# Kernel optimization log

Hardware: AMD Instinct MI355X
Metric: run time of the kernel (lower is better)

## Reference

```python
import jax, jax.numpy as jnp
import numpy as np

N, C, H, W = 64, 64, 8, 8   # batch, channels (img_net_out_dim), feature-map HxW
E = 256                      # ques_rnn_hidden_dim
G = 512                      # rn_g_dim
FD = 512                     # rn_f_dim
GIN = 2 * (C + 2) + E        # g-MLP input dim = 388
NUM_CLASSES = 2


def _lin(key, din, dout):
    # kaiming-uniform-like init for a Linear stored as (in, out)
    bound = float(np.sqrt(6.0 / din))
    w = jax.random.uniform(key, (din, dout), minval=-bound, maxval=bound, dtype=jnp.float32)
    b = jnp.zeros((dout,), dtype=jnp.float32)
    return w, b


def setup_inputs() -> dict:
    key = jax.random.key(0)
    ks = jax.random.split(key, 9)
    img = jax.random.normal(ks[0], (N, C, H, W), dtype=jnp.float32)
    ques = jax.random.normal(ks[1], (N, E), dtype=jnp.float32)
    g_w1, g_b1 = _lin(ks[2], GIN, G)
    g_w2, g_b2 = _lin(ks[3], G, G)
    g_w3, g_b3 = _lin(ks[4], G, G)
    g_w4, g_b4 = _lin(ks[5], G, G)
    f_w1, f_b1 = _lin(ks[6], G, FD)
    f_w2, f_b2 = _lin(ks[7], FD, FD)
    f_w3, f_b3 = _lin(ks[8], FD, NUM_CLASSES)
    return dict(img=img, ques=ques,
                g_w1=g_w1, g_b1=g_b1, g_w2=g_w2, g_b2=g_b2,
                g_w3=g_w3, g_b3=g_b3, g_w4=g_w4, g_b4=g_b4,
                f_w1=f_w1, f_b1=f_b1, f_w2=f_w2, f_b2=f_b2,
                f_w3=f_w3, f_b3=f_b3)


def _img_to_pairs(img, ques):
    # img: (n, c, h, w), ques: (n, e) -> pairs: (n, hw*hw, 2*(c+2)+e)
    n, c, h, w = img.shape
    hw = h * w
    cells = img.reshape(n, c, hw)
    idx = jnp.arange(hw)
    loc = jnp.stack([idx // w, idx % w], axis=0).astype(img.dtype)  # (2, hw)
    cells = jnp.concatenate([cells, jnp.broadcast_to(loc[None], (n, 2, hw))], axis=1)
    feats = cells.transpose(0, 2, 1)  # (n, hw, c+2)
    fdim = feats.shape[-1]
    one = jnp.broadcast_to(feats[:, :, None, :], (n, hw, hw, fdim))   # object i
    two = jnp.broadcast_to(feats[:, None, :, :], (n, hw, hw, fdim))   # object j
    q = jnp.broadcast_to(ques[:, None, None, :], (n, hw, hw, ques.shape[-1]))
    return jnp.concatenate([one, two, q], axis=-1).reshape(n, hw * hw, -1)


def reference(img, ques, g_w1, g_b1, g_w2, g_b2, g_w3, g_b3, g_w4, g_b4,
              f_w1, f_b1, f_w2, f_b2, f_w3, f_b3):
    pairs = _img_to_pairs(img, ques)                      # (N, HW^2, GIN)
    hdd = jax.nn.relu(pairs @ g_w1 + g_b1)                # shared g-MLP over all pairs
    hdd = jax.nn.relu(hdd @ g_w2 + g_b2)
    hdd = jax.nn.relu(hdd @ g_w3 + g_b3)
    hdd = jax.nn.relu(hdd @ g_w4 + g_b4)
    context = hdd.mean(axis=1)                            # (N, G)
    z = jax.nn.relu(context @ f_w1 + f_b1)                # f-MLP (dropout = identity in eval)
    z = jax.nn.relu(z @ f_w2 + f_b2)
    scores = z @ f_w3 + f_b3                              # (N, 2)
    return jax.nn.log_softmax(scores, axis=1)
```

## Files before the change

kernel.cpp:

```cpp
#include <hip/hip_runtime.h>

typedef unsigned short u16;
typedef unsigned int u32;
typedef _Float16 f16;

using half8 = __attribute__((ext_vector_type(8))) _Float16;
using f32x4 = __attribute__((ext_vector_type(4))) float;

__device__ __forceinline__ void async16(const void* g, void* l) {
    __builtin_amdgcn_global_load_lds(
        (const __attribute__((address_space(1))) u32*)g,
        (__attribute__((address_space(3))) u32*)l, 16, 0, 0);
}

__global__ __launch_bounds__(512) void prep_p12(const float* __restrict__ img,
                                                const float* __restrict__ gw1,
                                                float* __restrict__ P1,
                                                f16* __restrict__ P2h) {
    const int blk = blockIdx.x;
    const int n = blk >> 3;
    const int c0 = (blk & 7) * 8;
    const int t = threadIdx.x;
    __shared__ float feats[8][68];
    for (int idx = t; idx < 8 * 66; idx += 512) {
        int rr = idx / 66, cc = idx % 66, cell = c0 + rr;
        float v;
        if (cc < 64)       v = img[((size_t)(n * 64 + cc)) * 64 + cell];
        else if (cc == 64) v = (float)(cell >> 3);
        else               v = (float)(cell & 7);
        feats[rr][cc] = v;
    }
    __syncthreads();
    const int g = t;
    float a1[8], a2[8];
#pragma unroll
    for (int r = 0; r < 8; ++r) { a1[r] = 0.f; a2[r] = 0.f; }
    for (int c = 0; c < 66; ++c) {
        float wa = gw1[(size_t)c * 512 + g];
        float wb = gw1[(size_t)(66 + c) * 512 + g];
#pragma unroll
        for (int r = 0; r < 8; ++r) {
            a1[r] += feats[r][c] * wa;
            a2[r] += feats[r][c] * wb;
        }
    }
#pragma unroll
    for (int r = 0; r < 8; ++r) {
        P1[((size_t)(n * 64 + c0 + r)) * 512 + g] = a1[r];
        P2h[((size_t)(n * 64 + c0 + r)) * 512 + g] = (f16)a2[r];
    }
}

__global__ __launch_bounds__(512) void prep_q2(const float* __restrict__ ques,
                                               const float* __restrict__ gw1,
                                               const float* __restrict__ gb1,
                                               const float* __restrict__ P1,
                                               f16* __restrict__ P1h,
                                               float* __restrict__ Ctx) {
    const int n = blockIdx.x;
    const int t = threadIdx.x;
    __shared__ float q[256];
    if (t < 256) q[t] = ques[(size_t)n * 256 + t];
    __syncthreads();
    float acc = gb1[t];
    for (int e = 0; e < 256; ++e)
        acc += q[e] * gw1[(size_t)(132 + e) * 512 + t];
    const float* src = P1 + (((size_t)(n * 64)) << 9) + t;
    f16* dst = P1h + (((size_t)(n * 64)) << 9) + t;
    for (int r = 0; r < 64; ++r)
        dst[(size_t)r * 512] = (f16)(src[(size_t)r * 512] + acc);
    Ctx[(size_t)n * 512 + t] = 0.f;
}

__global__ void transpose_w(const float* __restrict__ W2, const float* __restrict__ W3,
                            const float* __restrict__ W4, f16* __restrict__ T2,
                            f16* __restrict__ T3, f16* __restrict__ T4) {
    const int L = blockIdx.z;
    const float* W = (L == 0) ? W2 : ((L == 1) ? W3 : W4);
    f16* T = (L == 0) ? T2 : ((L == 1) ? T3 : T4);
    __shared__ float tile[32][33];
    const int bx = blockIdx.x * 32;
    const int by = blockIdx.y * 32;
    const int tx = threadIdx.x, ty = threadIdx.y;
    for (int r = ty; r < 32; r += 8)
        tile[r][tx] = W[(size_t)(by + r) * 512 + bx + tx];
    __syncthreads();
    for (int r = ty; r < 32; r += 8)
        T[(size_t)(bx + r) * 512 + by + tx] = (f16)tile[tx][r];
}

__global__ __launch_bounds__(256, 2) void gemm2c(
    const f16* __restrict__ P1h, const f16* __restrict__ P2h,
    const f16* __restrict__ Bt, const float* __restrict__ bias,
    f16* __restrict__ Out, int row_base) {
    const int tid = threadIdx.x;
    const int lane = tid & 63;
    const int quad = lane >> 4;
    const int l15 = lane & 15;
    const int wv = tid >> 6;
    const int wm = wv >> 1, wn = wv & 1;
    const int b  = blockIdx.x;
    const int x  = b & 7;
    const int s  = b >> 3;
    const int bn = s & 3;
    const int bm = (s >> 2) * 8 + x;

    __shared__ alignas(16) f16 lA[2][256 * 32];
    __shared__ alignas(16) f16 lB[2][128 * 32];

    const int p0 = row_base + bm * 256;
    const int nb = p0 >> 12;
    const f16* P1b = P1h + (((size_t)(nb * 64)) << 9);
    const f16* P2b = P2h + (((size_t)(nb * 64)) << 9);

    auto stageB = [&](int kt, int buf) {
#pragma unroll
        for (int c = 0; c < 2; ++c) {
            int p = c * 256 + tid;
            int r = p >> 2;
            int g = ((p & 3) - (r >> 1)) & 3;
            const f16* srcB = Bt + (((size_t)(bn * 128 + r)) << 9) + kt * 32 + g * 8;
            async16(srcB, &lB[buf][(c * 256 + (tid & ~63)) * 8]);
        }
    };
    auto constructA = [&](int kt, int buf) {
#pragma unroll
        for (int c = 0; c < 4; ++c) {
            int p = c * 256 + tid;
            int r = p >> 2;
            int g = ((p & 3) - (r >> 1)) & 3;
            int k = kt * 32 + g * 8;
            int ii = ((bm * 4) + (r >> 6)) & 63;
            int jj = r & 63;
            half8 xx = *(const half8*)(P1b + (((size_t)ii) << 9) + k);
            half8 yy = *(const half8*)(P2b + (((size_t)jj) << 9) + k);
            half8 sv = xx + yy;
            sv = __builtin_elementwise_max(sv, (half8)(f16)0.f);
            *(half8*)&lA[buf][p * 8] = sv;
        }
    };

    f32x4 acc[8][4];
#pragma unroll
    for (int mi = 0; mi < 8; ++mi)
#pragma unroll
        for (int ni = 0; ni < 4; ++ni)
            acc[mi][ni] = (f32x4){0.f, 0.f, 0.f, 0.f};

    stageB(0, 0);
    constructA(0, 0);
    __syncthreads();

    for (int kt = 0; kt < 16; ++kt) {
        const int cur = kt & 1;
        if (kt < 15) {
            stageB(kt + 1, cur ^ 1);
            constructA(kt + 1, cur ^ 1);
        }
        half8 af[8], bf[4];
#pragma unroll
        for (int mi = 0; mi < 8; ++mi) {
            int r = wm * 128 + mi * 16 + l15;
            af[mi] = *(const half8*)&lA[cur][(r * 4 + ((quad + (r >> 1)) & 3)) * 8];
        }
#pragma unroll
        for (int ni = 0; ni < 4; ++ni) {
            int r = wn * 64 + ni * 16 + l15;
            bf[ni] = *(const half8*)&lB[cur][(r * 4 + ((quad + (r >> 1)) & 3)) * 8];
        }
#pragma unroll
        for (int mi = 0; mi < 8; ++mi)
#pragma unroll
            for (int ni = 0; ni < 4; ++ni)
                acc[mi][ni] = __builtin_amdgcn_mfma_f32_16x16x32_f16(
                    af[mi], bf[ni], acc[mi][ni], 0, 0, 0);
        __syncthreads();
    }

#pragma unroll
    for (int mi = 0; mi < 8; ++mi) {
#pragma unroll
        for (int ni = 0; ni < 4; ++ni) {
            int col = bn * 128 + wn * 64 + ni * 16 + l15;
            float bb = bias[col];
#pragma unroll
            for (int rr = 0; rr < 4; ++rr) {
                int row = bm * 256 + wm * 128 + mi * 16 + quad * 4 + rr;
                float v = fmaxf(acc[mi][ni][rr] + bb, 0.f);
                Out[(((size_t)row) << 9) + col] = (f16)v;
            }
        }
    }
}

template <bool REDUCE>
__global__ __launch_bounds__(256, 2) void gemm_kernel(
    const f16* __restrict__ Ain, const f16* __restrict__ Bt,
    const float* __restrict__ bias, f16* __restrict__ Out,
    float* __restrict__ Ctx, int row_base) {
    const int tid = threadIdx.x;
    const int lane = tid & 63;
    const int quad = lane >> 4;
    const int l15 = lane & 15;
    const int wv = tid >> 6;
    const int wm = wv >> 1, wn = wv & 1;
    const int b  = blockIdx.x;
    const int x  = b & 7;
    const int s  = b >> 3;
    const int bn = s & 3;
    const int bm = (s >> 2) * 8 + x;

    __shared__ alignas(16) f16 lA[256 * 64];
    __shared__ alignas(16) f16 lB[128 * 64];
    __shared__ float lsum[128];

    if (REDUCE && tid < 128) lsum[tid] = 0.f;

    f32x4 acc[8][4];
#pragma unroll
    for (int mi = 0; mi < 8; ++mi)
#pragma unroll
        for (int ni = 0; ni < 4; ++ni)
            acc[mi][ni] = (f32x4){0.f, 0.f, 0.f, 0.f};

    for (int kt = 0; kt < 8; ++kt) {
        const int k0 = kt * 64;
#pragma unroll
        for (int c = 0; c < 8; ++c) {
            int p = c * 256 + tid;
            int r = p >> 3;
            int gc = ((p & 7) - r) & 7;
            const f16* srcA = Ain + (((size_t)(bm * 256 + r)) << 9) + k0 + gc * 8;
            async16(srcA, &lA[(c * 256 + (tid & ~63)) * 8]);
        }
#pragma unroll
        for (int c = 0; c < 4; ++c) {
            int p = c * 256 + tid;
            int r = p >> 3;
            int gc = ((p & 7) - r) & 7;
            const f16* srcB = Bt + (((size_t)(bn * 128 + r)) << 9) + k0 + gc * 8;
            async16(srcB, &lB[(c * 256 + (tid & ~63)) * 8]);
        }
        __syncthreads();
#pragma unroll
        for (int ks = 0; ks < 2; ++ks) {
            half8 af[8], bf[4];
            const int gc = ks * 4 + quad;
#pragma unroll
            for (int mi = 0; mi < 8; ++mi) {
                int r = wm * 128 + mi * 16 + l15;
                af[mi] = *(const half8*)&lA[(r * 8 + ((gc + r) & 7)) * 8];
            }
#pragma unroll
            for (int ni = 0; ni < 4; ++ni) {
                int r = wn * 64 + ni * 16 + l15;
                bf[ni] = *(const half8*)&lB[(r * 8 + ((gc + r) & 7)) * 8];
            }
#pragma unroll
            for (int mi = 0; mi < 8; ++mi)
#pragma unroll
                for (int ni = 0; ni < 4; ++ni)
                    acc[mi][ni] = __builtin_amdgcn_mfma_f32_16x16x32_f16(
                        af[mi], bf[ni], acc[mi][ni], 0, 0, 0);
        }
        __syncthreads();
    }

    if (!REDUCE) {
#pragma unroll
        for (int mi = 0; mi < 8; ++mi) {
#pragma unroll
            for (int ni = 0; ni < 4; ++ni) {
                int col = bn * 128 + wn * 64 + ni * 16 + l15;
                float bb = bias[col];
#pragma unroll
                for (int rr = 0; rr < 4; ++rr) {
                    int row = bm * 256 + wm * 128 + mi * 16 + quad * 4 + rr;
                    float v = fmaxf(acc[mi][ni][rr] + bb, 0.f);
                    Out[(((size_t)row) << 9) + col] = (f16)v;
                }
            }
        }
    } else {
#pragma unroll
        for (int ni = 0; ni < 4; ++ni) {
            int coll = wn * 64 + ni * 16 + l15;
            float bb = bias[bn * 128 + coll];
            float ssum = 0.f;
#pragma unroll
            for (int mi = 0; mi < 8; ++mi)
#pragma unroll
                for (int rr = 0; rr < 4; ++rr)
                    ssum += fmaxf(acc[mi][ni][rr] + bb, 0.f);
            ssum += __shfl_xor(ssum, 16, 64);
            ssum += __shfl_xor(ssum, 32, 64);
            if (quad == 0) atomicAdd(&lsum[coll], ssum);
        }
        __syncthreads();
        if (tid < 128) {
            int nb = (row_base + bm * 256) >> 12;
            atomicAdd(&Ctx[(((size_t)nb) << 9) + bn * 128 + tid], lsum[tid]);
        }
    }
}

__global__ __launch_bounds__(512) void fmlp_layer(
    const float* __restrict__ In, const float* __restrict__ Wt,
    const float* __restrict__ bias, float* __restrict__ Out, float scale) {
    const int n = blockIdx.x, cs = blockIdx.y;
    const int t = threadIdx.x;
    const int col = cs * 64 + (t & 63);
    const int seg = t >> 6;
    __shared__ float a[512];
    __shared__ float red[512];
    a[t] = In[(size_t)n * 512 + t] * scale;
    __syncthreads();
    float p = 0.f;
#pragma unroll 8
    for (int i = seg * 64; i < seg * 64 + 64; ++i)
        p += a[i] * Wt[(size_t)i * 512 + col];
    red[t] = p;
    __syncthreads();
    if (t < 64) {
        float v = bias[col];
#pragma unroll
        for (int sg = 0; sg < 8; ++sg) v += red[sg * 64 + t];
        Out[(size_t)n * 512 + cs * 64 + t] = fmaxf(v, 0.f);
    }
}

__global__ __launch_bounds__(64) void fmlp_out(
    const float* __restrict__ A2, const float* __restrict__ fw3,
    const float* __restrict__ fb3, float* __restrict__ out) {
    const int n = blockIdx.x;
    const int lane = threadIdx.x;
    float s0 = 0.f, s1 = 0.f;
    for (int i = lane; i < 512; i += 64) {
        float v = A2[(size_t)n * 512 + i];
        s0 += v * fw3[i * 2];
        s1 += v * fw3[i * 2 + 1];
    }
#pragma unroll
    for (int d = 1; d < 64; d <<= 1) {
        s0 += __shfl_xor(s0, d, 64);
        s1 += __shfl_xor(s1, d, 64);
    }
    if (lane == 0) {
        s0 += fb3[0];
        s1 += fb3[1];
        float m = fmaxf(s0, s1);
        float l = logf(expf(s0 - m) + expf(s1 - m)) + m;
        out[n * 2 + 0] = s0 - l;
        out[n * 2 + 1] = s1 - l;
    }
}

extern "C" void kernel_launch(void* const* d_in, const int* in_sizes, int n_in,
                              void* d_out, int out_size, void* d_ws, size_t ws_size,
                              hipStream_t stream) {
    const float* img  = (const float*)d_in[0];
    const float* ques = (const float*)d_in[1];
    const float* gw1  = (const float*)d_in[2];
    const float* gb1  = (const float*)d_in[3];
    const float* gw2  = (const float*)d_in[4];
    const float* gb2  = (const float*)d_in[5];
    const float* gw3  = (const float*)d_in[6];
    const float* gb3  = (const float*)d_in[7];
    const float* gw4  = (const float*)d_in[8];
    const float* gb4  = (const float*)d_in[9];
    const float* fw1  = (const float*)d_in[10];
    const float* fb1  = (const float*)d_in[11];
    const float* fw2  = (const float*)d_in[12];
    const float* fb2  = (const float*)d_in[13];
    const float* fw3  = (const float*)d_in[14];
    const float* fb3  = (const float*)d_in[15];

    char* ws = (char*)d_ws;
    size_t off = 0;
    float* P1  = (float*)(ws + off); off += (size_t)4096 * 512 * 4;
    f16* P1h = (f16*)(ws + off); off += (size_t)4096 * 512 * 2;
    f16* P2h = (f16*)(ws + off); off += (size_t)4096 * 512 * 2;
    float* Ctx = (float*)(ws + off); off += (size_t)64 * 512 * 4;
    float* Z1  = (float*)(ws + off); off += (size_t)64 * 512 * 4;
    float* Z2  = (float*)(ws + off); off += (size_t)64 * 512 * 4;
    f16* T2 = (f16*)(ws + off); off += (size_t)512 * 512 * 2;
    f16* T3 = (f16*)(ws + off); off += (size_t)512 * 512 * 2;
    f16* T4 = (f16*)(ws + off); off += (size_t)512 * 512 * 2;
    const int MCH = 65536;
    f16* HA = (f16*)(ws + off); off += (size_t)MCH * 512 * 2;
    f16* HB = (f16*)(ws + off); off += (size_t)MCH * 512 * 2;

    prep_p12<<<512, 512, 0, stream>>>(img, gw1, P1, P2h);
    prep_q2<<<64, 512, 0, stream>>>(ques, gw1, gb1, P1, P1h, Ctx);
    transpose_w<<<dim3(16, 16, 3), dim3(32, 8), 0, stream>>>(gw2, gw3, gw4, T2, T3, T4);

    const int ggrid = (MCH / 256) * 4;
    for (int ch = 0; ch < 262144 / MCH; ++ch) {
        int row_base = ch * MCH;
        gemm2c<<<ggrid, 256, 0, stream>>>(P1h, P2h, T2, gb2, HB, row_base);
        gemm_kernel<false><<<ggrid, 256, 0, stream>>>(HB, T3, gb3, HA, nullptr, row_base);
        gemm_kernel<true ><<<ggrid, 256, 0, stream>>>(HA, T4, gb4, nullptr, Ctx, row_base);
    }

    fmlp_layer<<<dim3(64, 8), 512, 0, stream>>>(Ctx, fw1, fb1, Z1, 1.0f / 4096.0f);
    fmlp_layer<<<dim3(64, 8), 512, 0, stream>>>(Z1, fw2, fb2, Z2, 1.0f);
    fmlp_out<<<64, 64, 0, stream>>>(Z2, fw3, fb3, (float*)d_out);
}
```

Measured before the change: 577.5 us.

## Fuse g-MLP layers 2-4 into one kernel keeping activations in LDS

Replaces the chunked three-kernel GEMM pipeline with one fused kernel. Each 512-thread block owns 128 pair rows and keeps their full 512-wide activation in shared memory across layers 2, 3 and 4, so the f16 intermediates no longer round-trip through HBM. Weights are read straight from global memory into registers with a one-step prefetch, replacing the LDS-staged async loads. The 128 KB LDS tile limits occupancy to one block per CU, and weight reads now depend on cache hits, which may leave MFMA units starved.

```diff
diff --git a/kernel.cpp b/kernel.cpp
--- a/kernel.cpp
+++ b/kernel.cpp
@@ -6,12 +6,6 @@
 
 using half8 = __attribute__((ext_vector_type(8))) _Float16;
 using f32x4 = __attribute__((ext_vector_type(4))) float;
-
-__device__ __forceinline__ void async16(const void* g, void* l) {
-    __builtin_amdgcn_global_load_lds(
-        (const __attribute__((address_space(1))) u32*)g,
-        (__attribute__((address_space(3))) u32*)l, 16, 0, 0);
-}
 
 __global__ __launch_bounds__(512) void prep_p12(const float* __restrict__ img,
                                                 const float* __restrict__ gw1,
@@ -89,56 +83,39 @@
         T[(size_t)(bx + r) * 512 + by + tx] = (f16)tile[tx][r];
 }
 
-__global__ __launch_bounds__(256, 2) void gemm2c(
+__global__ __launch_bounds__(512, 2) void fused_g234(
     const f16* __restrict__ P1h, const f16* __restrict__ P2h,
-    const f16* __restrict__ Bt, const float* __restrict__ bias,
-    f16* __restrict__ Out, int row_base) {
+    const f16* __restrict__ T2, const f16* __restrict__ T3,
+    const f16* __restrict__ T4, const float* __restrict__ gb2,
+    const float* __restrict__ gb3, const float* __restrict__ gb4,
+    float* __restrict__ Ctx) {
     const int tid = threadIdx.x;
     const int lane = tid & 63;
     const int quad = lane >> 4;
     const int l15 = lane & 15;
     const int wv = tid >> 6;
-    const int wm = wv >> 1, wn = wv & 1;
-    const int b  = blockIdx.x;
-    const int x  = b & 7;
-    const int s  = b >> 3;
-    const int bn = s & 3;
-    const int bm = (s >> 2) * 8 + x;
-
-    __shared__ alignas(16) f16 lA[2][256 * 32];
-    __shared__ alignas(16) f16 lB[2][128 * 32];
-
-    const int p0 = row_base + bm * 256;
-    const int nb = p0 >> 12;
-    const f16* P1b = P1h + (((size_t)(nb * 64)) << 9);
+    const int b = blockIdx.x;
+    const int nb = b >> 5;
+    const int i0 = (b & 31) * 2;
+
+    __shared__ alignas(16) f16 H[128 * 512];
+
+    const f16* P1b = P1h + (((size_t)(nb * 64 + i0)) << 9);
     const f16* P2b = P2h + (((size_t)(nb * 64)) << 9);
 
-    auto stageB = [&](int kt, int buf) {
-#pragma unroll
-        for (int c = 0; c < 2; ++c) {
-            int p = c * 256 + tid;
-            int r = p >> 2;
-            int g = ((p & 3) - (r >> 1)) & 3;
-            const f16* srcB = Bt + (((size_t)(bn * 128 + r)) << 9) + kt * 32 + g * 8;
-            async16(srcB, &lB[buf][(c * 256 + (tid & ~63)) * 8]);
-        }
-    };
-    auto constructA = [&](int kt, int buf) {
-#pragma unroll
-        for (int c = 0; c < 4; ++c) {
-            int p = c * 256 + tid;
-            int r = p >> 2;
-            int g = ((p & 3) - (r >> 1)) & 3;
-            int k = kt * 32 + g * 8;
-            int ii = ((bm * 4) + (r >> 6)) & 63;
-            int jj = r & 63;
-            half8 xx = *(const half8*)(P1b + (((size_t)ii) << 9) + k);
-            half8 yy = *(const half8*)(P2b + (((size_t)jj) << 9) + k);
-            half8 sv = xx + yy;
-            sv = __builtin_elementwise_max(sv, (half8)(f16)0.f);
-            *(half8*)&lA[buf][p * 8] = sv;
-        }
-    };
+    {
+        const int k0 = lane * 8;
+#pragma unroll
+        for (int u = 0; u < 16; ++u) {
+            int r = u * 8 + wv;
+            half8 x = *(const half8*)(P1b + (((size_t)(r >> 6)) << 9) + k0);
+            half8 y = *(const half8*)(P2b + (((size_t)(r & 63)) << 9) + k0);
+            half8 s = x + y;
+            s = __builtin_elementwise_max(s, (half8)(f16)0.f);
+            *(half8*)&H[r * 512 + (k0 ^ ((wv & 7) << 3))] = s;
+        }
+    }
+    __syncthreads();
 
     f32x4 acc[8][4];
 #pragma unroll
@@ -147,115 +124,30 @@
         for (int ni = 0; ni < 4; ++ni)
             acc[mi][ni] = (f32x4){0.f, 0.f, 0.f, 0.f};
 
-    stageB(0, 0);
-    constructA(0, 0);
-    __syncthreads();
-
-    for (int kt = 0; kt < 16; ++kt) {
-        const int cur = kt & 1;
-        if (kt < 15) {
-            stageB(kt + 1, cur ^ 1);
-            constructA(kt + 1, cur ^ 1);
-        }
-        half8 af[8], bf[4];
-#pragma unroll
-        for (int mi = 0; mi < 8; ++mi) {
-            int r = wm * 128 + mi * 16 + l15;
-            af[mi] = *(const half8*)&lA[cur][(r * 4 + ((quad + (r >> 1)) & 3)) * 8];
-        }
-#pragma unroll
-        for (int ni = 0; ni < 4; ++ni) {
-            int r = wn * 64 + ni * 16 + l15;
-            bf[ni] = *(const half8*)&lB[cur][(r * 4 + ((quad + (r >> 1)) & 3)) * 8];
-        }
-#pragma unroll
-        for (int mi = 0; mi < 8; ++mi)
-#pragma unroll
-            for (int ni = 0; ni < 4; ++ni)
-                acc[mi][ni] = __builtin_amdgcn_mfma_f32_16x16x32_f16(
-                    af[mi], bf[ni], acc[mi][ni], 0, 0, 0);
-        __syncthreads();
-    }
-
-#pragma unroll
-    for (int mi = 0; mi < 8; ++mi) {
-#pragma unroll
-        for (int ni = 0; ni < 4; ++ni) {
-            int col = bn * 128 + wn * 64 + ni * 16 + l15;
-            float bb = bias[col];
-#pragma unroll
-            for (int rr = 0; rr < 4; ++rr) {
-                int row = bm * 256 + wm * 128 + mi * 16 + quad * 4 + rr;
-                float v = fmaxf(acc[mi][ni][rr] + bb, 0.f);
-                Out[(((size_t)row) << 9) + col] = (f16)v;
+    auto loadB = [&](const f16* __restrict__ T, int kt, int ni) -> half8 {
+        int col = wv * 64 + ni * 16 + l15;
+        return *(const half8*)(T + (((size_t)col) << 9) + kt * 32 + quad * 8);
+    };
+
+    auto run_layer = [&](const f16* __restrict__ T) {
+        half8 bfn[4];
+#pragma unroll
+        for (int ni = 0; ni < 4; ++ni) bfn[ni] = loadB(T, 0, ni);
+        const int swz = (l15 & 7) << 3;
+#pragma unroll 4
+        for (int kt = 0; kt < 16; ++kt) {
+            half8 bf[4];
+#pragma unroll
+            for (int ni = 0; ni < 4; ++ni) bf[ni] = bfn[ni];
+            if (kt < 15) {
+#pragma unroll
+                for (int ni = 0; ni < 4; ++ni) bfn[ni] = loadB(T, kt + 1, ni);
             }
-        }
-    }
-}
-
-template <bool REDUCE>
-__global__ __launch_bounds__(256, 2) void gemm_kernel(
-    const f16* __restrict__ Ain, const f16* __restrict__ Bt,
-    const float* __restrict__ bias, f16* __restrict__ Out,
-    float* __restrict__ Ctx, int row_base) {
-    const int tid = threadIdx.x;
-    const int lane = tid & 63;
-    const int quad = lane >> 4;
-    const int l15 = lane & 15;
-    const int wv = tid >> 6;
-    const int wm = wv >> 1, wn = wv & 1;
-    const int b  = blockIdx.x;
-    const int x  = b & 7;
-    const int s  = b >> 3;
-    const int bn = s & 3;
-    const int bm = (s >> 2) * 8 + x;
-
-    __shared__ alignas(16) f16 lA[256 * 64];
-    __shared__ alignas(16) f16 lB[128 * 64];
-    __shared__ float lsum[128];
-
-    if (REDUCE && tid < 128) lsum[tid] = 0.f;
-
-    f32x4 acc[8][4];
-#pragma unroll
-    for (int mi = 0; mi < 8; ++mi)
-#pragma unroll
-        for (int ni = 0; ni < 4; ++ni)
-            acc[mi][ni] = (f32x4){0.f, 0.f, 0.f, 0.f};
-
-    for (int kt = 0; kt < 8; ++kt) {
-        const int k0 = kt * 64;
-#pragma unroll
-        for (int c = 0; c < 8; ++c) {
-            int p = c * 256 + tid;
-            int r = p >> 3;
-            int gc = ((p & 7) - r) & 7;
-            const f16* srcA = Ain + (((size_t)(bm * 256 + r)) << 9) + k0 + gc * 8;
-            async16(srcA, &lA[(c * 256 + (tid & ~63)) * 8]);
-        }
-#pragma unroll
-        for (int c = 0; c < 4; ++c) {
-            int p = c * 256 + tid;
-            int r = p >> 3;
-            int gc = ((p & 7) - r) & 7;
-            const f16* srcB = Bt + (((size_t)(bn * 128 + r)) << 9) + k0 + gc * 8;
-            async16(srcB, &lB[(c * 256 + (tid & ~63)) * 8]);
-        }
-        __syncthreads();
-#pragma unroll
-        for (int ks = 0; ks < 2; ++ks) {
-            half8 af[8], bf[4];
-            const int gc = ks * 4 + quad;
-#pragma unroll
-            for (int mi = 0; mi < 8; ++mi) {
-                int r = wm * 128 + mi * 16 + l15;
-                af[mi] = *(const half8*)&lA[(r * 8 + ((gc + r) & 7)) * 8];
-            }
-#pragma unroll
-            for (int ni = 0; ni < 4; ++ni) {
-                int r = wn * 64 + ni * 16 + l15;
-                bf[ni] = *(const half8*)&lB[(r * 8 + ((gc + r) & 7)) * 8];
-            }
+            const int kb = (kt * 32 + quad * 8) ^ swz;
+            half8 af[8];
+#pragma unroll
+            for (int mi = 0; mi < 8; ++mi)
+                af[mi] = *(const half8*)&H[(mi * 16 + l15) * 512 + kb];
 #pragma unroll
             for (int mi = 0; mi < 8; ++mi)
 #pragma unroll
@@ -263,44 +155,50 @@
                     acc[mi][ni] = __builtin_amdgcn_mfma_f32_16x16x32_f16(
                         af[mi], bf[ni], acc[mi][ni], 0, 0, 0);
         }
+    };
+
+    auto writeback = [&](const float* __restrict__ bias) {
+        float bb[4];
+#pragma unroll
+        for (int ni = 0; ni < 4; ++ni)
+            bb[ni] = bias[wv * 64 + ni * 16 + l15];
         __syncthreads();
-    }
-
-    if (!REDUCE) {
 #pragma unroll
         for (int mi = 0; mi < 8; ++mi) {
 #pragma unroll
             for (int ni = 0; ni < 4; ++ni) {
-                int col = bn * 128 + wn * 64 + ni * 16 + l15;
-                float bb = bias[col];
+                int col = wv * 64 + ni * 16 + l15;
 #pragma unroll
                 for (int rr = 0; rr < 4; ++rr) {
-                    int row = bm * 256 + wm * 128 + mi * 16 + quad * 4 + rr;
-                    float v = fmaxf(acc[mi][ni][rr] + bb, 0.f);
-                    Out[(((size_t)row) << 9) + col] = (f16)v;
+                    int row = mi * 16 + quad * 4 + rr;
+                    float v = fmaxf(acc[mi][ni][rr] + bb[ni], 0.f);
+                    H[row * 512 + (col ^ ((row & 7) << 3))] = (f16)v;
+                    acc[mi][ni][rr] = 0.f;
                 }
             }
         }
-    } else {
-#pragma unroll
-        for (int ni = 0; ni < 4; ++ni) {
-            int coll = wn * 64 + ni * 16 + l15;
-            float bb = bias[bn * 128 + coll];
-            float ssum = 0.f;
-#pragma unroll
-            for (int mi = 0; mi < 8; ++mi)
-#pragma unroll
-                for (int rr = 0; rr < 4; ++rr)
-                    ssum += fmaxf(acc[mi][ni][rr] + bb, 0.f);
-            ssum += __shfl_xor(ssum, 16, 64);
-            ssum += __shfl_xor(ssum, 32, 64);
-            if (quad == 0) atomicAdd(&lsum[coll], ssum);
-        }
         __syncthreads();
-        if (tid < 128) {
-            int nb = (row_base + bm * 256) >> 12;
-            atomicAdd(&Ctx[(((size_t)nb) << 9) + bn * 128 + tid], lsum[tid]);
-        }
+    };
+
+    run_layer(T2);
+    writeback(gb2);
+    run_layer(T3);
+    writeback(gb3);
+    run_layer(T4);
+
+#pragma unroll
+    for (int ni = 0; ni < 4; ++ni) {
+        float bb = gb4[wv * 64 + ni * 16 + l15];
+        float s = 0.f;
+#pragma unroll
+        for (int mi = 0; mi < 8; ++mi)
+#pragma unroll
+            for (int rr = 0; rr < 4; ++rr)
+                s += fmaxf(acc[mi][ni][rr] + bb, 0.f);
+        s += __shfl_xor(s, 16, 64);
+        s += __shfl_xor(s, 32, 64);
+        if (quad == 0)
+            atomicAdd(&Ctx[(((size_t)nb) << 9) + wv * 64 + ni * 16 + l15], s);
     }
 }
 
@@ -386,21 +284,12 @@
     f16* T2 = (f16*)(ws + off); off += (size_t)512 * 512 * 2;
     f16* T3 = (f16*)(ws + off); off += (size_t)512 * 512 * 2;
     f16* T4 = (f16*)(ws + off); off += (size_t)512 * 512 * 2;
-    const int MCH = 65536;
-    f16* HA = (f16*)(ws + off); off += (size_t)MCH * 512 * 2;
-    f16* HB = (f16*)(ws + off); off += (size_t)MCH * 512 * 2;
 
     prep_p12<<<512, 512, 0, stream>>>(img, gw1, P1, P2h);
     prep_q2<<<64, 512, 0, stream>>>(ques, gw1, gb1, P1, P1h, Ctx);
     transpose_w<<<dim3(16, 16, 3), dim3(32, 8), 0, stream>>>(gw2, gw3, gw4, T2, T3, T4);
 
-    const int ggrid = (MCH / 256) * 4;
-    for (int ch = 0; ch < 262144 / MCH; ++ch) {
-        int row_base = ch * MCH;
-        gemm2c<<<ggrid, 256, 0, stream>>>(P1h, P2h, T2, gb2, HB, row_base);
-        gemm_kernel<false><<<ggrid, 256, 0, stream>>>(HB, T3, gb3, HA, nullptr, row_base);
-        gemm_kernel<true ><<<ggrid, 256, 0, stream>>>(HA, T4, gb4, nullptr, Ctx, row_base);
-    }
+    fused_g234<<<2048, 512, 0, stream>>>(P1h, P2h, T2, T3, T4, gb2, gb3, gb4, Ctx);
 
     fmlp_layer<<<dim3(64, 8), 512, 0, stream>>>(Ctx, fw1, fb1, Z1, 1.0f / 4096.0f);
     fmlp_layer<<<dim3(64, 8), 512, 0, stream>>>(Z1, fw2, fb2, Z2, 1.0f);
```

Measured after the change: 750.0 us. 29.9% more time.
